# Kernel optimization log

Hardware: AMD Instinct MI355X
Metric: run time of the kernel (lower is better)

Reference implementation:

```python
import jax, jax.numpy as jnp
import numpy as np

NUM_HEADS = 8


def _conv3x3(x, w, b):
    # x: (B, C, H, W); w: (O, I, 3, 3) -> (B, O, H, W), stride 1, SAME padding
    y = jax.lax.conv_general_dilated(
        x, w, window_strides=(1, 1), padding='SAME',
        dimension_numbers=('NCHW', 'OIHW', 'NCHW'))
    return y + b[None, :, None, None]


def setup_inputs() -> dict:
    key = jax.random.key(0)
    ks = jax.random.split(key, 7)
    bs, mc, C, H, W = 2, 5, 640, 32, 32
    s = 0.02  # init scale for weights
    return {
        'x': jax.random.normal(ks[0], (bs, mc, C, H, W), jnp.float32),
        'wq': jax.random.normal(ks[1], (C, C, 3, 3), jnp.float32) * s,
        'bq': jnp.zeros((C,), jnp.float32),
        'wk': jax.random.normal(ks[2], (C, C, 3, 3), jnp.float32) * s,
        'bk': jnp.zeros((C,), jnp.float32),
        'wv': jax.random.normal(ks[3], (C, C, 3, 3), jnp.float32) * s,
        'bv': jnp.zeros((C,), jnp.float32),
        'w_proj': jax.random.normal(ks[4], (C, C), jnp.float32) * s,
        'b_proj': jnp.zeros((C,), jnp.float32),
    }


def reference(x, wq, bq, wk, bk, wv, bv, w_proj, b_proj):
    bs, mc, C, H, W = x.shape
    N = H * W
    nh = NUM_HEADS
    hd = C // nh
    scale = hd ** -0.5

    xf = x.reshape(bs * mc, C, H, W)

    def proj(w, b):
        # conv -> (bs, mc, nh, hd, N) -> (bs, mc, nh, N, hd)
        y = _conv3x3(xf, w, b).reshape(bs, mc, nh, hd, N)
        return y.transpose(0, 1, 2, 4, 3)

    q = proj(wq, bq)
    k = proj(wk, bk)
    v = proj(wv, bv)

    attn = jax.nn.softmax(jnp.einsum('bmhnd,bmhkd->bmhnk', q, k) * scale, axis=-1)
    o = jnp.einsum('bmhnk,bmhkd->bmhnd', attn, v)  # (bs, mc, nh, N, hd)

    # permute(0,3,1,2,4).reshape(bs, N, mc*C) then split back to (bs, N, mc, C)
    o = o.transpose(0, 3, 1, 2, 4).reshape(bs, N, mc, C)
    o = jnp.einsum('bnmc,dc->bnmd', o, w_proj) + b_proj  # Linear(C, C)
    return o.reshape(bs, N, mc * C)
```

## Files before the change

### kernel.cpp

```cpp
#include <hip/hip_runtime.h>

typedef _Float16 half_t;
typedef _Float16 half8 __attribute__((ext_vector_type(8)));
typedef _Float16 half4 __attribute__((ext_vector_type(4)));
typedef float floatx4 __attribute__((ext_vector_type(4)));
typedef unsigned int u32;

#define MFMA32(a,b,c) __builtin_amdgcn_mfma_f32_16x16x32_f16(a,b,c,0,0,0)
#define MFMA16(a,b,c) __builtin_amdgcn_mfma_f32_16x16x16f16(a,b,c,0,0,0)

#define XPAD_ELEMS (10u*34*34*640)
#define WR_ELEMS   (3u*9*640*640)
#define WP_ELEMS   (640u*640)
#define QKV_ELEMS  (10u*8*1024*80)
#define O_ELEMS    (10u*1024*640)

__device__ __forceinline__ void load16_lds(half_t* lds, const half_t* g) {
  __builtin_amdgcn_global_load_lds((const __attribute__((address_space(1))) u32*)g,
                                   (__attribute__((address_space(3))) u32*)lds,
                                   16, 0, 0);
}

__global__ __launch_bounds__(256) void k_convert_x(const float* __restrict__ x,
                                                   half_t* __restrict__ xpad) {
  const int img = blockIdx.x >> 5, y = blockIdx.x & 31;
  const float* src = x + (size_t)img*640*1024 + y*32;
  half_t* dst = xpad + (size_t)img*34*34*640;
  for (int i = threadIdx.x; i < 640*32; i += 256) {
    int xx = i / 640, c = i - xx*640;
    float v = src[(size_t)c*1024 + xx];
    dst[((size_t)(y+1)*34 + xx + 1)*640 + c] = (half_t)v;
  }
}

__global__ __launch_bounds__(256) void k_convert_w(const float* __restrict__ wq,
                                                   const float* __restrict__ wk,
                                                   const float* __restrict__ wv,
                                                   const float* __restrict__ wp,
                                                   half_t* __restrict__ wr2,
                                                   half_t* __restrict__ wp16) {
  __shared__ half_t tr[9*644];
  const int p = blockIdx.y, row = blockIdx.x;
  if (p < 3) {
    const float* W = (p == 0) ? wq : (p == 1) ? wk : wv;
    const float* src = W + (size_t)row*5760;
    for (int j = threadIdx.x; j < 5760; j += 256) {
      int ci = j / 9, t = j - ci*9;
      tr[t*644 + ci] = (half_t)src[j];
    }
    __syncthreads();
    half_t* dst = wr2 + ((size_t)p*640 + row)*5760;
    for (int i = threadIdx.x; i < 5760; i += 256) {
      int t = i / 640, ci = i - t*640;
      dst[i] = tr[t*644 + ci];
    }
  } else {
    for (int i = threadIdx.x; i < 640; i += 256)
      wp16[(size_t)row*640 + i] = (half_t)wp[(size_t)row*640 + i];
  }
}

#define TRC(T) (((T)/3)*34 + ((T) - ((T)/3)*3))
#define K0C(T) ((((T)+2)%9)*640 + (((T)+2)/9)*32)

__global__ __launch_bounds__(512) void k_conv(const half_t* __restrict__ xpad,
                                              const half_t* __restrict__ wr2,
                                              const float* __restrict__ bq,
                                              const float* __restrict__ bk,
                                              const float* __restrict__ bv,
                                              half_t* __restrict__ qo,
                                              half_t* __restrict__ ko,
                                              half_t* __restrict__ vo) {
  __shared__ __align__(16) half_t sX[2][1536*8];
  __shared__ __align__(16) half_t sW[3][640*8];
  const int tid = threadIdx.x;
  const int lane = tid & 63, wv = tid >> 6;
  const int l15 = lane & 15, lq = lane >> 4, lq16 = lq*16;
  const int id = blockIdx.x;
  const int wg = (id >> 3) + (id & 7)*60;
  const int mt = wg & 3;
  const int rest = wg >> 2;
  const int nt = rest & 3;
  const int z  = rest >> 2;
  const int proj = z / 10, img = z - proj*10;

  const half_t* xg  = xpad + ((size_t)img*34*34 + (size_t)mt*8*34)*640;
  const half_t* wgp = wr2 + ((size_t)proj*640 + nt*160)*5760;

  int xsrc[3];
#pragma unroll
  for (int kk = 0; kk < 3; ++kk) {
    int unit = kk*512 + tid;
    int row = unit >> 2, sub = unit & 3;
    int ch = sub ^ ((row >> 1) & 3);
    xsrc[kk] = row*640 + ch*8;
  }
  int wsrc0, wsrc1;
  { int row = tid >> 2, sub = tid & 3;
    int ch = sub ^ ((row >> 1) & 3);
    wsrc0 = row*5760 + ch*8; }
  { int unit = 512 + tid;
    int row = unit >> 2, sub = unit & 3;
    int ch = sub ^ ((row >> 1) & 3);
    wsrc1 = row*5760 + ch*8; }

  const int wm = wv >> 1, wn = wv & 1;
  int arow0[4];
#pragma unroll
  for (int fr = 0; fr < 4; ++fr) {
    int p = wm*64 + fr*16 + l15;
    arow0[fr] = (p >> 5)*34 + (p & 31);
  }
  int bbase;
  { int r = wn*80 + l15;
    bbase = r*64 + (lq16 ^ (((r >> 1) & 3) << 4)); }

#pragma unroll
  for (int kk = 0; kk < 3; ++kk)
    load16_lds(sX[0] + (size_t)(kk*512 + wv*64)*8, xg + xsrc[kk]);
  load16_lds(sW[0] + (size_t)(wv*64)*8, wgp + wsrc0);
  if (wv < 2) load16_lds(sW[0] + (size_t)(512 + wv*64)*8, wgp + wsrc1);
  load16_lds(sW[1] + (size_t)(wv*64)*8, wgp + wsrc0 + 640);
  if (wv < 2) load16_lds(sW[1] + (size_t)(512 + wv*64)*8, wgp + wsrc1 + 640);
  if (wv < 2) asm volatile("s_waitcnt vmcnt(2)" ::: "memory");
  else        asm volatile("s_waitcnt vmcnt(1)" ::: "memory");
  asm volatile("s_barrier" ::: "memory");

  floatx4 acc[4][5] = {};

#define STEP1(T, DOW, K0E, DOX, VMW)                                               \
  do {                                                                             \
    half8 Av0, Aw0, Aw1, Aw2, Aw3, Aw4;                                            \
    { const char* sXc = (const char*)sxr;                                          \
      const char* sWc = (const char*)(sW[(T)%3]);                                  \
      int r0 = arow0[0] + TRC(T);                                                  \
      Av0 = *(const half8*)(sXc + r0*64 + (lq16 ^ (((r0>>1)&3)<<4)));              \
      Aw0 = *(const half8*)(sWc + bbase);                                          \
      Aw1 = *(const half8*)(sWc + bbase + 1024);                                   \
      Aw2 = *(const half8*)(sWc + bbase + 2048);                                   \
      Aw3 = *(const half8*)(sWc + bbase + 3072);                                   \
      Aw4 = *(const half8*)(sWc + bbase + 4096); }                                 \
    if (DOW) {                                                                     \
      load16_lds(sW[((T)+2)%3] + (size_t)(wv*64)*8, wgp + wsrc0 + (K0E));          \
      if (wv < 2)                                                                  \
        load16_lds(sW[((T)+2)%3] + (size_t)(512 + wv*64)*8, wgp + wsrc1 + (K0E));  \
    }                                                                              \
    if (DOX) {                                                                     \
      _Pragma("unroll")                                                            \
      for (int kk = 0; kk < 3; ++kk)                                               \
        load16_lds(sxw + (size_t)(kk*512 + wv*64)*8, xg + xsrc[kk] + (g+1)*32);    \
    }                                                                              \
    if ((VMW) == 2) {                                                              \
      if (wv < 2) asm volatile("s_waitcnt vmcnt(5)" ::: "memory");                 \
      else        asm volatile("s_waitcnt vmcnt(4)" ::: "memory");                 \
    } else if ((VMW) == 1) {                                                       \
      if (wv < 2) asm volatile("s_waitcnt vmcnt(2)" ::: "memory");                 \
      else        asm volatile("s_waitcnt vmcnt(1)" ::: "memory");                 \
    } else {                                                                       \
      asm volatile("s_waitcnt vmcnt(0)" ::: "memory");                             \
    }                                                                              \
    asm volatile("s_waitcnt lgkmcnt(0)" ::: "memory");                             \
    asm volatile("s_barrier" ::: "memory");                                        \
    __builtin_amdgcn_sched_barrier(0);                                             \
    __builtin_amdgcn_s_setprio(1);                                                 \
    { const char* sXc = (const char*)sxr;                                          \
      int r1 = arow0[1] + TRC(T);                                                  \
      half8 Av1 = *(const half8*)(sXc + r1*64 + (lq16 ^ (((r1>>1)&3)<<4)));        \
      acc[0][0] = MFMA32(Av0, Aw0, acc[0][0]);                                     \
      acc[0][1] = MFMA32(Av0, Aw1, acc[0][1]);                                     \
      acc[0][2] = MFMA32(Av0, Aw2, acc[0][2]);                                     \
      int r2 = arow0[2] + TRC(T);                                                  \
      half8 Av2 = *(const half8*)(sXc + r2*64 + (lq16 ^ (((r2>>1)&3)<<4)));        \
      acc[0][3] = MFMA32(Av0, Aw3, acc[0][3]);                                     \
      acc[0][4] = MFMA32(Av0, Aw4, acc[0][4]);                                     \
      int r3 = arow0[3] + TRC(T);                                                  \
      half8 Av3 = *(const half8*)(sXc + r3*64 + (lq16 ^ (((r3>>1)&3)<<4)));        \
      acc[1][0] = MFMA32(Av1, Aw0, acc[1][0]);                                     \
      acc[1][1] = MFMA32(Av1, Aw1, acc[1][1]);                                     \
      acc[1][2] = MFMA32(Av1, Aw2, acc[1][2]);                                     \
      acc[1][3] = MFMA32(Av1, Aw3, acc[1][3]);                                     \
      acc[1][4] = MFMA32(Av1, Aw4, acc[1][4]);                                     \
      acc[2][0] = MFMA32(Av2, Aw0, acc[2][0]);                                     \
      acc[2][1] = MFMA32(Av2, Aw1, acc[2][1]);                                     \
      acc[2][2] = MFMA32(Av2, Aw2, acc[2][2]);                                     \
      acc[2][3] = MFMA32(Av2, Aw3, acc[2][3]);                                     \
      acc[2][4] = MFMA32(Av2, Aw4, acc[2][4]);                                     \
      acc[3][0] = MFMA32(Av3, Aw0, acc[3][0]);                                     \
      acc[3][1] = MFMA32(Av3, Aw1, acc[3][1]);                                     \
      acc[3][2] = MFMA32(Av3, Aw2, acc[3][2]);                                     \
      acc[3][3] = MFMA32(Av3, Aw3, acc[3][3]);                                     \
      acc[3][4] = MFMA32(Av3, Aw4, acc[3][4]);                                     \
    }                                                                              \
    __builtin_amdgcn_s_setprio(0);                                                 \
  } while (0)

  for (int g = 0; g < 19; ++g) {
    half_t* sxr = sX[g & 1];
    half_t* sxw = sX[(g + 1) & 1];
    STEP1(0, 1, K0C(0) + g*32, 0, 1);
    STEP1(1, 1, K0C(1) + g*32, 0, 1);
    STEP1(2, 1, K0C(2) + g*32, 0, 1);
    STEP1(3, 1, K0C(3) + g*32, 0, 1);
    STEP1(4, 1, K0C(4) + g*32, 0, 1);
    STEP1(5, 1, K0C(5) + g*32, 0, 1);
    STEP1(6, 1, K0C(6) + g*32, 1, 2);
    STEP1(7, 1, K0C(7) + g*32, 0, 2);
    STEP1(8, 1, K0C(8) + g*32, 0, 1);
  }
  {
    const int g = 19;
    half_t* sxr = sX[1];
    half_t* sxw = sX[0];
    (void)sxw;
    STEP1(0, 1, K0C(0) + 19*32, 0, 1);
    STEP1(1, 1, K0C(1) + 19*32, 0, 1);
    STEP1(2, 1, K0C(2) + 19*32, 0, 1);
    STEP1(3, 1, K0C(3) + 19*32, 0, 1);
    STEP1(4, 1, K0C(4) + 19*32, 0, 1);
    STEP1(5, 1, K0C(5) + 19*32, 0, 1);
    STEP1(6, 1, K0C(6) + 19*32, 0, 1);
    STEP1(7, 0, 0, 0, 0);
    STEP1(8, 0, 0, 0, 0);
    (void)g;
  }
#undef STEP1

  const float* bias = (proj == 0) ? bq : (proj == 1) ? bk : bv;
#pragma unroll
  for (int fc = 0; fc < 5; ++fc) {
    int co = nt*160 + wn*80 + fc*16 + l15;
    float bb = bias[co];
    int hh = 2*nt + wn;
    int d  = fc*16 + l15;
#pragma unroll
    for (int fr = 0; fr < 4; ++fr)
#pragma unroll
      for (int j = 0; j < 4; ++j) {
        int n = mt*256 + wm*64 + fr*16 + lq*4 + j;
        float val = acc[fr][fc][j] + bb;
        if (proj == 0)      qo[((size_t)(img*8 + hh)*1024 + n)*80 + d] = (half_t)(val * 0.11180339887498949f);
        else if (proj == 1) ko[((size_t)(img*8 + hh)*1024 + n)*80 + d] = (half_t)val;
        else                vo[((size_t)(img*8 + hh)*80 + d)*1024 + n] = (half_t)val;
      }
  }
}

__global__ __launch_bounds__(256) void k_attn(const half_t* __restrict__ qg_,
                                              const half_t* __restrict__ kg_,
                                              const half_t* __restrict__ vg_,
                                              half_t* __restrict__ og_) {
  __shared__ __align__(16) half_t sQ[128*80];
  __shared__ __align__(16) half_t sK[2][64*80];
  __shared__ __align__(16) half_t sV[2][80*64];
  __shared__ __align__(16) half_t sP[128*64];
  const int tid = threadIdx.x, lane = tid & 63, wv = tid >> 6;
  const int l15 = lane & 15, lq = lane >> 4;
  const int id = blockIdx.x;
  const int wgb = (id >> 3) + (id & 7)*80;
  const int qt = wgb & 7, gh = wgb >> 3;
  const half_t* qg = qg_ + ((size_t)gh*1024 + qt*128)*80;
  const half_t* kg = kg_ + (size_t)gh*1024*80;
  const half_t* vg = vg_ + (size_t)gh*80*1024;

#define STAGE_KV(kt, buf) do {                                                \
    _Pragma("unroll")                                                         \
    for (int kk = 0; kk < 3; ++kk) {                                          \
      int c = kk*256 + tid;                                                   \
      if (c < 640) {                                                          \
        int row = c / 10, cw = c - row*10;                                    \
        load16_lds(sK[buf] + (size_t)(kk*256 + wv*64)*8,                      \
                   kg + ((size_t)(kt)*64 + row)*80 + cw*8);                   \
      }                                                                       \
    }                                                                         \
    _Pragma("unroll")                                                         \
    for (int kk = 0; kk < 3; ++kk) {                                          \
      int c = kk*256 + tid;                                                   \
      if (c < 640) {                                                          \
        load16_lds(sV[buf] + (size_t)(kk*256 + wv*64)*8,                      \
                   vg + (size_t)(c >> 3)*1024 + (kt)*64 + (c & 7)*8);         \
      }                                                                       \
    }                                                                         \
  } while (0)

#pragma unroll
  for (int kk = 0; kk < 5; ++kk)
    load16_lds(sQ + (size_t)(kk*256 + wv*64)*8, qg + (size_t)(kk*256 + tid)*8);
  STAGE_KV(0, 0);
  asm volatile("s_waitcnt vmcnt(0)" ::: "memory");
  __builtin_amdgcn_s_barrier();
  __builtin_amdgcn_sched_barrier(0);

  half8 qa0[2], qa1[2]; half4 qa2[2];
  {
    const char* sQb = (const char*)sQ;
#pragma unroll
    for (int fr = 0; fr < 2; ++fr) {
      int r = wv*32 + fr*16 + l15;
      qa0[fr] = *(const half8*)(sQb + r*160 + lq*16);
      qa1[fr] = *(const half8*)(sQb + r*160 + 64 + lq*16);
      qa2[fr] = *(const half4*)(sQb + r*160 + 128 + lq*8);
    }
  }

  float mrow[2][4], lrow[2][4];
  floatx4 oacc[2][5] = {};
#pragma unroll
  for (int fr = 0; fr < 2; ++fr)
#pragma unroll
    for (int j = 0; j < 4; ++j) { mrow[fr][j] = -1e30f; lrow[fr][j] = 0.f; }

  for (int kt = 0; kt < 16; ++kt) {
    const int cur = kt & 1;
    if (kt < 15) STAGE_KV(kt + 1, cur ^ 1);

    const char* sKb = (const char*)sK[cur];
    floatx4 s[2][4];
#pragma unroll
    for (int fc = 0; fc < 4; ++fc) {
      int key = fc*16 + l15;
      half8 kb0 = *(const half8*)(sKb + key*160 + lq*16);
      half8 kb1 = *(const half8*)(sKb + key*160 + 64 + lq*16);
      half4 kb2 = *(const half4*)(sKb + key*160 + 128 + lq*8);
#pragma unroll
      for (int fr = 0; fr < 2; ++fr) {
        floatx4 t = {0.f, 0.f, 0.f, 0.f};
        t = MFMA16(qa2[fr], kb2, t);
        t = MFMA32(qa0[fr], kb0, t);
        t = MFMA32(qa1[fr], kb1, t);
        s[fr][fc] = t;
      }
    }

    float corr[2][4], psum[2][4];
#pragma unroll
    for (int fr = 0; fr < 2; ++fr)
#pragma unroll
      for (int j = 0; j < 4; ++j) {
        float mx = fmaxf(fmaxf(s[fr][0][j], s[fr][1][j]), fmaxf(s[fr][2][j], s[fr][3][j]));
        mx = fmaxf(mx, __shfl_xor(mx, 1));
        mx = fmaxf(mx, __shfl_xor(mx, 2));
        mx = fmaxf(mx, __shfl_xor(mx, 4));
        mx = fmaxf(mx, __shfl_xor(mx, 8));
        float mn = fmaxf(mrow[fr][j], mx);
        corr[fr][j] = __expf(mrow[fr][j] - mn);
        mrow[fr][j] = mn;
        psum[fr][j] = 0.f;
      }
#pragma unroll
    for (int fc = 0; fc < 4; ++fc)
#pragma unroll
      for (int fr = 0; fr < 2; ++fr)
#pragma unroll
        for (int j = 0; j < 4; ++j) {
          float p = __expf(s[fr][fc][j] - mrow[fr][j]);
          psum[fr][j] += p;
          sP[(size_t)(wv*32 + fr*16 + lq*4 + j)*64 + fc*16 + l15] = (half_t)p;
        }
#pragma unroll
    for (int fr = 0; fr < 2; ++fr)
#pragma unroll
      for (int j = 0; j < 4; ++j) {
        float t2 = psum[fr][j];
        t2 += __shfl_xor(t2, 1);
        t2 += __shfl_xor(t2, 2);
        t2 += __shfl_xor(t2, 4);
        t2 += __shfl_xor(t2, 8);
        lrow[fr][j] = lrow[fr][j]*corr[fr][j] + t2;
      }
#pragma unroll
    for (int fr = 0; fr < 2; ++fr)
#pragma unroll
      for (int fc = 0; fc < 5; ++fc)
#pragma unroll
        for (int j = 0; j < 4; ++j)
          oacc[fr][fc][j] *= corr[fr][j];

    asm volatile("s_waitcnt lgkmcnt(0)" ::: "memory");
    __builtin_amdgcn_s_barrier();
    __builtin_amdgcn_sched_barrier(0);

    const char* sPb = (const char*)sP;
    const char* sVb = (const char*)sV[cur];
    half8 pa[2][2];
#pragma unroll
    for (int fr = 0; fr < 2; ++fr) {
      int r = wv*32 + fr*16 + l15;
#pragma unroll
      for (int ks = 0; ks < 2; ++ks)
        pa[fr][ks] = *(const half8*)(sPb + r*128 + ks*64 + lq*16);
    }
#pragma unroll
    for (int fc = 0; fc < 5; ++fc)
#pragma unroll
      for (int ks = 0; ks < 2; ++ks) {
        half8 vb = *(const half8*)(sVb + (fc*16 + l15)*128 + ks*64 + lq*16);
#pragma unroll
        for (int fr = 0; fr < 2; ++fr)
          oacc[fr][fc] = MFMA32(pa[fr][ks], vb, oacc[fr][fc]);
      }

    asm volatile("s_waitcnt vmcnt(0) lgkmcnt(0)" ::: "memory");
    __builtin_amdgcn_s_barrier();
    __builtin_amdgcn_sched_barrier(0);
  }
#undef STAGE_KV

  const int img = gh >> 3, hh = gh & 7;
  half_t* og = og_ + ((size_t)img*1024 + qt*128)*640 + hh*80;
#pragma unroll
  for (int fr = 0; fr < 2; ++fr)
#pragma unroll
    for (int j = 0; j < 4; ++j) {
      int n = wv*32 + fr*16 + lq*4 + j;
      float inv = 1.f / lrow[fr][j];
#pragma unroll
      for (int fc = 0; fc < 5; ++fc)
        og[(size_t)n*640 + fc*16 + l15] = (half_t)(oacc[fr][fc][j] * inv);
    }
}

__global__ __launch_bounds__(256) void k_proj(const half_t* __restrict__ oa,
                                              const half_t* __restrict__ wp,
                                              const float* __restrict__ bp,
                                              float* __restrict__ out) {
  __shared__ __align__(16) half_t sA[128*32];
  __shared__ __align__(16) half_t sB[128*32];
  const int tid = threadIdx.x, lane = tid & 63, wv = tid >> 6;
  const int l15 = lane & 15, lq = lane >> 4;
  const int mt = blockIdx.x, nt = blockIdx.y, img = blockIdx.z;
  const int bb = img / 5, mm = img - bb*5;
  const half_t* ag = oa + ((size_t)img*1024 + mt*128)*640;
  const half_t* bg = wp + (size_t)nt*128*640;
  const int wrow = (wv >> 1)*64, wcol = (wv & 1)*64;
  floatx4 acc[4][4] = {};
  for (int g = 0; g < 20; ++g) {
    __syncthreads();
#pragma unroll
    for (int kk = 0; kk < 2; ++kk) {
      int c = kk*256 + tid;
      load16_lds(sA + (size_t)(kk*256 + wv*64)*8, ag + (size_t)(c >> 2)*640 + g*32 + (c & 3)*8);
      load16_lds(sB + (size_t)(kk*256 + wv*64)*8, bg + (size_t)(c >> 2)*640 + g*32 + (c & 3)*8);
    }
    __syncthreads();
    const char* sAb = (const char*)sA;
    const char* sBb = (const char*)sB;
    half8 av[4], bw[4];
#pragma unroll
    for (int fr = 0; fr < 4; ++fr) av[fr] = *(const half8*)(sAb + (wrow + fr*16 + l15)*64 + lq*16);
#pragma unroll
    for (int fc = 0; fc < 4; ++fc) bw[fc] = *(const half8*)(sBb + (wcol + fc*16 + l15)*64 + lq*16);
#pragma unroll
    for (int fr = 0; fr < 4; ++fr)
#pragma unroll
      for (int fc = 0; fc < 4; ++fc)
        acc[fr][fc] = MFMA32(av[fr], bw[fc], acc[fr][fc]);
  }
  float* og = out + ((size_t)bb*1024 + mt*128)*3200 + mm*640 + nt*128;
#pragma unroll
  for (int fc = 0; fc < 4; ++fc) {
    float bias = bp[nt*128 + wcol + fc*16 + l15];
#pragma unroll
    for (int fr = 0; fr < 4; ++fr)
#pragma unroll
      for (int j = 0; j < 4; ++j)
        og[(size_t)(wrow + fr*16 + lq*4 + j)*3200 + wcol + fc*16 + l15] = acc[fr][fc][j] + bias;
  }
}

extern "C" void kernel_launch(void* const* d_in, const int* in_sizes, int n_in,
                              void* d_out, int out_size, void* d_ws, size_t ws_size,
                              hipStream_t stream) {
  const float* x  = (const float*)d_in[0];
  const float* wq = (const float*)d_in[1];
  const float* bq = (const float*)d_in[2];
  const float* wk = (const float*)d_in[3];
  const float* bk = (const float*)d_in[4];
  const float* wv = (const float*)d_in[5];
  const float* bv = (const float*)d_in[6];
  const float* wp = (const float*)d_in[7];
  const float* bp = (const float*)d_in[8];
  float* out = (float*)d_out;

  half_t* xpad = (half_t*)d_ws;
  half_t* wr2  = xpad + XPAD_ELEMS;
  half_t* wp16 = wr2 + WR_ELEMS;
  half_t* q    = wp16 + WP_ELEMS;
  half_t* k    = q + QKV_ELEMS;
  half_t* v    = k + QKV_ELEMS;
  half_t* oa   = v + QKV_ELEMS;

  (void)hipMemsetAsync(xpad, 0, (size_t)XPAD_ELEMS*sizeof(half_t), stream);
  k_convert_x<<<320, 256, 0, stream>>>(x, xpad);
  k_convert_w<<<dim3(640, 4), 256, 0, stream>>>(wq, wk, wv, wp, wr2, wp16);
  k_conv<<<480, 512, 0, stream>>>(xpad, wr2, bq, bk, bv, q, k, v);
  k_attn<<<640, 256, 0, stream>>>(q, k, v, oa);
  k_proj<<<dim3(8, 5, 10), 256, 0, stream>>>(oa, wp16, bp, out);
}
```

Baseline: 398.2 us.

## Pipeline proj GEMM with triple buffering, swizzle LDS, transpose x via LDS

The projection GEMM now uses a three-slot LDS ring with async prefetch two K-steps ahead, an XOR swizzle to cut LDS bank conflicts, and a remapped 1D grid that groups blocks for cache locality. The input conversion kernel transposes through shared memory so global reads and writes are both coalesced. The attention kernel loads Q straight from global memory into registers instead of staging it through LDS, which frees LDS. Together these aim to hide memory latency and reduce bank conflicts, at the cost of more LDS in the projection kernel and hand-tuned waitcnt logic that must stay correct.

```diff
diff --git a/kernel.cpp b/kernel.cpp
--- a/kernel.cpp
+++ b/kernel.cpp
@@ -23,14 +23,18 @@
 
 __global__ __launch_bounds__(256) void k_convert_x(const float* __restrict__ x,
                                                    half_t* __restrict__ xpad) {
+  __shared__ half_t tr[32*644];
   const int img = blockIdx.x >> 5, y = blockIdx.x & 31;
   const float* src = x + (size_t)img*640*1024 + y*32;
-  half_t* dst = xpad + (size_t)img*34*34*640;
+  half_t* dst = xpad + ((size_t)img*34*34 + (size_t)(y+1)*34 + 1)*640;
   for (int i = threadIdx.x; i < 640*32; i += 256) {
-    int xx = i / 640, c = i - xx*640;
-    float v = src[(size_t)c*1024 + xx];
-    dst[((size_t)(y+1)*34 + xx + 1)*640 + c] = (half_t)v;
-  }
+    int xx = i & 31, c = i >> 5;
+    tr[xx*644 + c] = (half_t)src[(size_t)c*1024 + xx];
+  }
+  __syncthreads();
+  for (int xx = 0; xx < 32; ++xx)
+    for (int c = threadIdx.x; c < 640; c += 256)
+      dst[(size_t)xx*640 + c] = tr[xx*644 + c];
 }
 
 __global__ __launch_bounds__(256) void k_convert_w(const float* __restrict__ wq,
@@ -249,7 +253,6 @@
                                               const half_t* __restrict__ kg_,
                                               const half_t* __restrict__ vg_,
                                               half_t* __restrict__ og_) {
-  __shared__ __align__(16) half_t sQ[128*80];
   __shared__ __align__(16) half_t sK[2][64*80];
   __shared__ __align__(16) half_t sV[2][80*64];
   __shared__ __align__(16) half_t sP[128*64];
@@ -282,25 +285,18 @@
     }                                                                         \
   } while (0)
 
-#pragma unroll
-  for (int kk = 0; kk < 5; ++kk)
-    load16_lds(sQ + (size_t)(kk*256 + wv*64)*8, qg + (size_t)(kk*256 + tid)*8);
+  half8 qa0[2], qa1[2]; half4 qa2[2];
+#pragma unroll
+  for (int fr = 0; fr < 2; ++fr) {
+    int r = wv*32 + fr*16 + l15;
+    qa0[fr] = *(const half8*)(qg + (size_t)r*80 + lq*8);
+    qa1[fr] = *(const half8*)(qg + (size_t)r*80 + 32 + lq*8);
+    qa2[fr] = *(const half4*)(qg + (size_t)r*80 + 64 + lq*4);
+  }
   STAGE_KV(0, 0);
   asm volatile("s_waitcnt vmcnt(0)" ::: "memory");
   __builtin_amdgcn_s_barrier();
   __builtin_amdgcn_sched_barrier(0);
-
-  half8 qa0[2], qa1[2]; half4 qa2[2];
-  {
-    const char* sQb = (const char*)sQ;
-#pragma unroll
-    for (int fr = 0; fr < 2; ++fr) {
-      int r = wv*32 + fr*16 + l15;
-      qa0[fr] = *(const half8*)(sQb + r*160 + lq*16);
-      qa1[fr] = *(const half8*)(sQb + r*160 + 64 + lq*16);
-      qa2[fr] = *(const half4*)(sQb + r*160 + 128 + lq*8);
-    }
-  }
 
   float mrow[2][4], lrow[2][4];
   floatx4 oacc[2][5] = {};
@@ -423,38 +419,80 @@
                                               const half_t* __restrict__ wp,
                                               const float* __restrict__ bp,
                                               float* __restrict__ out) {
-  __shared__ __align__(16) half_t sA[128*32];
-  __shared__ __align__(16) half_t sB[128*32];
+  __shared__ __align__(16) half_t sA[3][128*32];
+  __shared__ __align__(16) half_t sB[3][128*32];
   const int tid = threadIdx.x, lane = tid & 63, wv = tid >> 6;
-  const int l15 = lane & 15, lq = lane >> 4;
-  const int mt = blockIdx.x, nt = blockIdx.y, img = blockIdx.z;
+  const int l15 = lane & 15, lq = lane >> 4, lq16 = lq*16;
+  const int id = blockIdx.x;
+  const int wg = (id >> 3) + (id & 7)*50;
+  const int mt = wg & 7;
+  const int rest = wg >> 3;
+  const int nt = rest % 5;
+  const int img = rest / 5;
   const int bb = img / 5, mm = img - bb*5;
   const half_t* ag = oa + ((size_t)img*1024 + mt*128)*640;
   const half_t* bg = wp + (size_t)nt*128*640;
   const int wrow = (wv >> 1)*64, wcol = (wv & 1)*64;
+
+  int asrc[2];
+#pragma unroll
+  for (int kk = 0; kk < 2; ++kk) {
+    int idx = kk*256 + tid;
+    int row = idx >> 2, sub = idx & 3;
+    int ch = sub ^ ((row >> 1) & 3);
+    asrc[kk] = row*640 + ch*8;
+  }
+
+#define STAGE_P(g, slot) do {                                                 \
+    _Pragma("unroll")                                                         \
+    for (int kk = 0; kk < 2; ++kk) {                                          \
+      load16_lds(sA[slot] + (size_t)(kk*256 + wv*64)*8, ag + asrc[kk] + (g)*32); \
+      load16_lds(sB[slot] + (size_t)(kk*256 + wv*64)*8, bg + asrc[kk] + (g)*32); \
+    }                                                                         \
+  } while (0)
+
+  STAGE_P(0, 0);
+  STAGE_P(1, 1);
+  asm volatile("s_waitcnt vmcnt(4)" ::: "memory");
+  asm volatile("s_barrier" ::: "memory");
+
   floatx4 acc[4][4] = {};
+  int aoff[4], boff[4];
+#pragma unroll
+  for (int fr = 0; fr < 4; ++fr) {
+    int r = wrow + fr*16 + l15;
+    aoff[fr] = (r << 6) + (lq16 ^ (((r >> 1) & 3) << 4));
+  }
+#pragma unroll
+  for (int fc = 0; fc < 4; ++fc) {
+    int r = wcol + fc*16 + l15;
+    boff[fc] = (r << 6) + (lq16 ^ (((r >> 1) & 3) << 4));
+  }
+
   for (int g = 0; g < 20; ++g) {
-    __syncthreads();
-#pragma unroll
-    for (int kk = 0; kk < 2; ++kk) {
-      int c = kk*256 + tid;
-      load16_lds(sA + (size_t)(kk*256 + wv*64)*8, ag + (size_t)(c >> 2)*640 + g*32 + (c & 3)*8);
-      load16_lds(sB + (size_t)(kk*256 + wv*64)*8, bg + (size_t)(c >> 2)*640 + g*32 + (c & 3)*8);
-    }
-    __syncthreads();
-    const char* sAb = (const char*)sA;
-    const char* sBb = (const char*)sB;
+    const int slot = g % 3;
+    if (g + 2 < 20) STAGE_P(g + 2, (g + 2) % 3);
+    const char* sAb = (const char*)sA[slot];
+    const char* sBb = (const char*)sB[slot];
     half8 av[4], bw[4];
 #pragma unroll
-    for (int fr = 0; fr < 4; ++fr) av[fr] = *(const half8*)(sAb + (wrow + fr*16 + l15)*64 + lq*16);
-#pragma unroll
-    for (int fc = 0; fc < 4; ++fc) bw[fc] = *(const half8*)(sBb + (wcol + fc*16 + l15)*64 + lq*16);
+    for (int fr = 0; fr < 4; ++fr) av[fr] = *(const half8*)(sAb + aoff[fr]);
+#pragma unroll
+    for (int fc = 0; fc < 4; ++fc) bw[fc] = *(const half8*)(sBb + boff[fc]);
 #pragma unroll
     for (int fr = 0; fr < 4; ++fr)
 #pragma unroll
       for (int fc = 0; fc < 4; ++fc)
         acc[fr][fc] = MFMA32(av[fr], bw[fc], acc[fr][fc]);
-  }
+    if (g < 19) {
+      if (g + 2 < 20) asm volatile("s_waitcnt vmcnt(4)" ::: "memory");
+      else            asm volatile("s_waitcnt vmcnt(0)" ::: "memory");
+      asm volatile("s_waitcnt lgkmcnt(0)" ::: "memory");
+      asm volatile("s_barrier" ::: "memory");
+    }
+  }
+#undef STAGE_P
+
   float* og = out + ((size_t)bb*1024 + mt*128)*3200 + mm*640 + nt*128;
 #pragma unroll
   for (int fc = 0; fc < 4; ++fc) {
@@ -494,5 +532,5 @@
   k_convert_w<<<dim3(640, 4), 256, 0, stream>>>(wq, wk, wv, wp, wr2, wp16);
   k_conv<<<480, 512, 0, stream>>>(xpad, wr2, bq, bk, bv, q, k, v);
   k_attn<<<640, 256, 0, stream>>>(q, k, v, oa);
-  k_proj<<<dim3(8, 5, 10), 256, 0, stream>>>(oa, wp16, bp, out);
-}
+  k_proj<<<400, 256, 0, stream>>>(oa, wp16, bp, out);
+}
```

Result: faster. 373.8 us, median of 2 (-6.1%).
